# Performance work log

Measured on AMD Instinct MI355X. Metric: run time of the kernel, lower is better.

Reference implementation:

```python
import jax, jax.numpy as jnp
import numpy as np

N, E, B = 20000, 100000, 16
U_SZ, U_RED = 4096, 256
EDGE_H, EDGE_OUT = 1024, 512
NODE_H = 512
X_DIM, EA_DIM = 9, 1


def _lin(key, fan_out, fan_in):
    kw, kb = jax.random.split(key)
    s = 1.0 / np.sqrt(fan_in)
    w = jax.random.uniform(kw, (fan_out, fan_in), jnp.float32, -s, s)
    b = jax.random.uniform(kb, (fan_out,), jnp.float32, -s, s)
    return w, b


def setup_inputs() -> dict:
    key = jax.random.key(0)
    ks = jax.random.split(key, 16)
    inp = {}
    inp["x"] = jax.random.normal(ks[0], (N, X_DIM), jnp.float32)
    inp["edge_index"] = jax.random.randint(ks[1], (2, E), 0, N, jnp.int64)
    inp["edge_attr"] = jax.random.normal(ks[2], (E, EA_DIM), jnp.float32)
    inp["u"] = jax.random.normal(ks[3], (B, U_SZ), jnp.float32)
    inp["batch"] = jnp.sort(jax.random.randint(ks[4], (N,), 0, B, jnp.int64))
    # select_dim_reduction: Linear(4096, 256)
    inp["w_sel"], inp["b_sel"] = _lin(ks[5], U_RED, U_SZ)
    # edge MLP: 275 -> 1024 -> 1024 -> 1024 -> 1024 -> 512
    e_in = EA_DIM + 2 * X_DIM + U_RED  # 275
    inp["ew0"], inp["eb0"] = _lin(ks[6], EDGE_H, e_in)
    inp["ew1"], inp["eb1"] = _lin(ks[7], EDGE_H, EDGE_H)
    inp["ew2"], inp["eb2"] = _lin(ks[8], EDGE_H, EDGE_H)
    inp["ew3"], inp["eb3"] = _lin(ks[9], EDGE_H, EDGE_H)
    inp["ew4"], inp["eb4"] = _lin(ks[10], EDGE_OUT, EDGE_H)
    # node_mlp_1: (9+512) -> 512 -> 512 (relu after each)
    inp["nw0"], inp["nb0"] = _lin(ks[11], NODE_H, X_DIM + EDGE_OUT)
    inp["nw1"], inp["nb1"] = _lin(ks[12], NODE_H, NODE_H)
    # node_mlp_2: (9+512+256) -> 512 -> 1
    inp["mw0"], inp["mb0"] = _lin(ks[13], NODE_H, X_DIM + NODE_H + U_RED)
    inp["mw1"], inp["mb1"] = _lin(ks[14], 1, NODE_H)
    return inp


def reference(x, edge_index, edge_attr, u, batch,
              w_sel, b_sel,
              ew0, eb0, ew1, eb1, ew2, eb2, ew3, eb3, ew4, eb4,
              nw0, nb0, nw1, nb1, mw0, mb0, mw1, mb1):
    row, col = edge_index[0], edge_index[1]
    u_r = u @ w_sel.T + b_sel                       # [B, 256]
    eb_idx = batch[row]                             # edge -> graph
    # EdgeModel: cat([src, dest, edge_attr, u[batch]]) -> MLP
    e_in = jnp.concatenate([x[row], x[col], edge_attr, u_r[eb_idx]], axis=1)  # [E,275]
    h = jax.nn.relu(e_in @ ew0.T + eb0)
    h = jax.nn.relu(h @ ew1.T + eb1)
    h = jax.nn.relu(h @ ew2.T + eb2)
    h = jax.nn.relu(h @ ew3.T + eb3)
    edge_out = h @ ew4.T + eb4                      # [E, 512]
    # NodeModel: gather x[col], edge MLP, scatter_mean onto row
    n_in = jnp.concatenate([x[col], edge_out], axis=1)  # [E, 521]
    h = jax.nn.relu(n_in @ nw0.T + nb0)
    h = jax.nn.relu(h @ nw1.T + nb1)                # [E, 512]
    seg_sum = jax.ops.segment_sum(h, row, num_segments=x.shape[0])
    cnt = jax.ops.segment_sum(jnp.ones((h.shape[0],), h.dtype), row, num_segments=x.shape[0])
    agg = seg_sum / jnp.maximum(cnt, 1.0)[:, None]  # scatter_mean
    m_in = jnp.concatenate([x, agg, u_r[batch]], axis=1)  # [N, 777]
    h2 = jax.nn.relu(m_in @ mw0.T + mb0)
    out = h2 @ mw1.T + mb1                          # [N, 1]
    return jnp.squeeze(out)
```

## Files before the change

### kernel.cpp

```cpp
#include <hip/hip_runtime.h>


#define NN 20000
#define EE 100000
#define BB 16

typedef _Float16 f16x8 __attribute__((ext_vector_type(8)));
typedef _Float16 f16x4 __attribute__((ext_vector_type(4)));
typedef float f32x4 __attribute__((ext_vector_type(4)));

__device__ __forceinline__ int clampi(int v, int hi) {
    return v < 0 ? 0 : (v >= hi ? hi - 1 : v);
}

__device__ __forceinline__ void gld_lds16(const void* g, void* l) {
    __builtin_amdgcn_global_load_lds(
        (const __attribute__((address_space(1))) unsigned int*)g,
        (__attribute__((address_space(3))) unsigned int*)l, 16, 0, 0);
}

__global__ __launch_bounds__(512, 2) void gemm256(
    const _Float16* __restrict__ Ag, const _Float16* __restrict__ Wt,
    int KT, int KTs, const float* __restrict__ bias,
    _Float16* __restrict__ C, int KTo, int ktOff)
{
    __shared__ _Float16 As[32768];
    __shared__ _Float16 Bs[32768];

    const int tid  = threadIdx.x;
    const int lane = tid & 63;
    const int wid  = tid >> 6;
    const int wm = wid & 1;
    const int wn = wid >> 1;
    const int l15 = lane & 15;
    const int l4  = (lane >> 4) << 2;

    const int nb = gridDim.x;
    const int MT2 = gridDim.y;
    int f = blockIdx.y * nb + blockIdx.x;
    const int MT8 = MT2 & ~7;
    int p, c;
    if (f < MT8 * nb) {
        c = (f >> 3) % nb;
        p = (f & 7) + 8 * ((f >> 3) / nb);
    } else {
        int g = f - MT8 * nb;
        p = MT8 + g / nb;
        c = g % nb;
    }

    const int KTT = KT >> 1;
    const size_t soff = (size_t)tid * 8;
    const int doff = (tid & ~63) * 8;
    const int aoff = wm * 4096 + ((lane >> 4) << 10) + l15 * 8;
    const int boff = (wn >> 1) * 4096 + ((lane >> 4) << 10)
                   + ((wn & 1) * 64 + l15) * 8;

    auto stageA = [&](int tn, int s) {
        const size_t kk = (size_t)(2 * tn + s);
        const _Float16* g0 = Ag + ((size_t)(2 * p)     * KTs + kk) * 4096 + soff;
        const _Float16* g1 = Ag + ((size_t)(2 * p + 1) * KTs + kk) * 4096 + soff;
        _Float16* d = As + ((tn & 1) << 14) + (s << 13) + doff;
        gld_lds16(g0, d);
        gld_lds16(g1, d + 4096);
    };
    auto stageB = [&](int tn, int s) {
        const size_t kk = (size_t)(2 * tn + s);
        const _Float16* g0 = Wt + ((size_t)(2 * c)     * KT + kk) * 4096 + soff;
        const _Float16* g1 = Wt + ((size_t)(2 * c + 1) * KT + kk) * 4096 + soff;
        _Float16* d = Bs + ((tn & 1) << 14) + (s << 13) + doff;
        gld_lds16(g0, d);
        gld_lds16(g1, d + 4096);
    };

    f32x4 acc[8][4];
#pragma unroll
    for (int i = 0; i < 8; ++i)
#pragma unroll
        for (int j = 0; j < 4; ++j) acc[i][j] = (f32x4){0.f, 0.f, 0.f, 0.f};

    stageA(0, 0); stageB(0, 0); stageA(0, 1); stageB(0, 1);

    for (int t = 0; t < KTT; ++t) {
        const int pb = (t & 1) << 14;
#pragma unroll
        for (int sub = 0; sub < 2; ++sub) {
            if (t == KTT - 1 && sub == 1)
                asm volatile("s_waitcnt vmcnt(0)" ::: "memory");
            else
                asm volatile("s_waitcnt vmcnt(4)" ::: "memory");
            __builtin_amdgcn_s_barrier();
            const _Float16* Asub = As + pb + (sub << 13) + aoff;
            const _Float16* Bsub = Bs + pb + (sub << 13) + boff;
            f16x8 af[4], bf[4];
#pragma unroll
            for (int j = 0; j < 4; ++j) bf[j] = *(const f16x8*)(Bsub + j * 128);
#pragma unroll
            for (int i = 0; i < 4; ++i) af[i] = *(const f16x8*)(Asub + i * 128);
            if (t + 1 < KTT) stageA(t + 1, sub);
            __builtin_amdgcn_s_setprio(1);
#pragma unroll
            for (int i = 0; i < 4; ++i)
#pragma unroll
                for (int j = 0; j < 4; ++j)
                    acc[i][j] = __builtin_amdgcn_mfma_f32_16x16x32_f16(
                        af[i], bf[j], acc[i][j], 0, 0, 0);
            __builtin_amdgcn_s_setprio(0);
            __builtin_amdgcn_s_barrier();
#pragma unroll
            for (int i = 0; i < 4; ++i)
                af[i] = *(const f16x8*)(Asub + (4 + i) * 128);
            if (t + 1 < KTT) stageB(t + 1, sub);
            __builtin_amdgcn_s_setprio(1);
#pragma unroll
            for (int i = 0; i < 4; ++i)
#pragma unroll
                for (int j = 0; j < 4; ++j)
                    acc[4 + i][j] = __builtin_amdgcn_mfma_f32_16x16x32_f16(
                        af[i], bf[j], acc[4 + i][j], 0, 0, 0);
            __builtin_amdgcn_s_setprio(0);
        }
    }

    _Float16* tr = As;
#pragma unroll
    for (int pass = 0; pass < 4; ++pass) {
        __syncthreads();
        if (wm == (pass >> 1)) {
            const int fi = (pass & 1) << 2;
#pragma unroll
            for (int i = 0; i < 4; ++i) {
#pragma unroll
                for (int v = 0; v < 4; ++v) {
                    const int lr = i * 16 + l4 + v;
#pragma unroll
                    for (int j = 0; j < 4; ++j) {
                        const int cc = wn * 64 + j * 16 + l15;
                        float val = acc[fi + i][j][v] + bias[c * 256 + cc];
                        val = fmaxf(val, 0.f);
                        tr[lr * 264 + cc] = (_Float16)val;
                    }
                }
            }
        }
        __syncthreads();
#pragma unroll
        for (int it = 0; it < 4; ++it) {
            const int id = it * 512 + tid;
            const int r  = id & 63;
            const int cg = id >> 6;
            f16x8 v8 = *(const f16x8*)(tr + r * 264 + cg * 8);
            const int kt = ktOff + c * 8 + (cg >> 2);
            const int mt_out = 2 * p + (pass >> 1);
            const int r128 = ((pass & 1) << 6) + r;
            *(f16x8*)(C + (((size_t)mt_out * KTo + kt) * 4 + (cg & 3)) * 1024
                        + (size_t)r128 * 8) = v8;
        }
    }
}

template <int MODE>
__global__ __launch_bounds__(256, 4) void gemm_blk(
    const _Float16* __restrict__ A,
    const _Float16* __restrict__ Wt,
    int KT, int KTs,
    const float* __restrict__ bias, int ldbias, const int* __restrict__ gbid,
    void* __restrict__ C, int KTo, int ktOff,
    int ldc,
    const int* __restrict__ srow, float* __restrict__ aux,
    int M, int relu)
{
    __shared__ char smem[32768];
    _Float16* As = (_Float16*)smem;
    _Float16* Bs = As + 8192;

    const int tid  = threadIdx.x;
    const int lane = tid & 63;
    const int wid  = tid >> 6;
    const int wm = (wid & 1) << 6;
    const int wn = (wid >> 1) << 6;

    const int nb = gridDim.x;
    const int MT = gridDim.y;
    int f = blockIdx.y * nb + blockIdx.x;
    const int MT8 = MT & ~7;
    int p, c;
    if (f < MT8 * nb) {
        c = (f >> 3) % nb;
        p = (f & 7) + 8 * ((f >> 3) / nb);
    } else {
        int g = f - MT8 * nb;
        p = MT8 + g / nb;
        c = g % nb;
    }

    f32x4 acc[4][4];
#pragma unroll
    for (int i = 0; i < 4; ++i)
#pragma unroll
        for (int j = 0; j < 4; ++j) acc[i][j] = (f32x4){0.f, 0.f, 0.f, 0.f};

    const _Float16* pA = A + (size_t)p * KTs * 4096;
    const _Float16* pB = Wt + (size_t)c * KT * 4096;
    const int cb0 = wid * 64;
    const int cb1 = 256 + wid * 64;
    const int kq  = (lane >> 4) * 128;
    const int l15 = lane & 15;
    const int l4  = (lane >> 4) << 2;

    int kt = 0;
    for (; kt + 2 <= KT; kt += 2) {
        __syncthreads();
        gld_lds16(pA + (size_t)(cb0 + lane) * 8,        As + cb0 * 8);
        gld_lds16(pA + (size_t)(cb1 + lane) * 8,        As + cb1 * 8);
        gld_lds16(pA + 4096 + (size_t)(cb0 + lane) * 8, As + 4096 + cb0 * 8);
        gld_lds16(pA + 4096 + (size_t)(cb1 + lane) * 8, As + 4096 + cb1 * 8);
        gld_lds16(pB + (size_t)(cb0 + lane) * 8,        Bs + cb0 * 8);
        gld_lds16(pB + (size_t)(cb1 + lane) * 8,        Bs + cb1 * 8);
        gld_lds16(pB + 4096 + (size_t)(cb0 + lane) * 8, Bs + 4096 + cb0 * 8);
        gld_lds16(pB + 4096 + (size_t)(cb1 + lane) * 8, Bs + 4096 + cb1 * 8);
        pA += 8192; pB += 8192;
        __syncthreads();

#pragma unroll
        for (int s = 0; s < 2; ++s) {
            f16x8 af[4], bf[4];
            const int sb = s * 4096;
#pragma unroll
            for (int i = 0; i < 4; ++i)
                af[i] = *(const f16x8*)(As + sb + (size_t)((kq + wm + i * 16 + l15) << 3));
#pragma unroll
            for (int j = 0; j < 4; ++j)
                bf[j] = *(const f16x8*)(Bs + sb + (size_t)((kq + wn + j * 16 + l15) << 3));
#pragma unroll
            for (int i = 0; i < 4; ++i)
#pragma unroll
                for (int j = 0; j < 4; ++j)
                    acc[i][j] = __builtin_amdgcn_mfma_f32_16x16x32_f16(af[i], bf[j], acc[i][j], 0, 0, 0);
        }
    }
    if (kt < KT) {
        __syncthreads();
        gld_lds16(pA + (size_t)(cb0 + lane) * 8, As + cb0 * 8);
        gld_lds16(pA + (size_t)(cb1 + lane) * 8, As + cb1 * 8);
        gld_lds16(pB + (size_t)(cb0 + lane) * 8, Bs + cb0 * 8);
        gld_lds16(pB + (size_t)(cb1 + lane) * 8, Bs + cb1 * 8);
        __syncthreads();
        f16x8 af[4], bf[4];
#pragma unroll
        for (int i = 0; i < 4; ++i)
            af[i] = *(const f16x8*)(As + (size_t)((kq + wm + i * 16 + l15) << 3));
#pragma unroll
        for (int j = 0; j < 4; ++j)
            bf[j] = *(const f16x8*)(Bs + (size_t)((kq + wn + j * 16 + l15) << 3));
#pragma unroll
        for (int i = 0; i < 4; ++i)
#pragma unroll
            for (int j = 0; j < 4; ++j)
                acc[i][j] = __builtin_amdgcn_mfma_f32_16x16x32_f16(af[i], bf[j], acc[i][j], 0, 0, 0);
    }

    if (MODE == 0) {
        _Float16* tr = (_Float16*)smem;
#pragma unroll
        for (int pass = 0; pass < 2; ++pass) {
            __syncthreads();
            if (wm == pass * 64) {
#pragma unroll
                for (int i = 0; i < 4; ++i) {
#pragma unroll
                    for (int v = 0; v < 4; ++v) {
                        const int lr = i * 16 + l4 + v;
                        const float* brow = bias;
                        if (gbid) {
                            int m = p * 128 + pass * 64 + lr;
                            if (m >= M) m = M - 1;
                            brow = bias + (size_t)clampi(gbid[m], BB) * ldbias;
                        }
#pragma unroll
                        for (int j = 0; j < 4; ++j) {
                            const int cc = wn + j * 16 + l15;
                            float val = acc[i][j][v] + brow[c * 128 + cc];
                            if (relu) val = fmaxf(val, 0.f);
                            tr[lr * 132 + cc] = (_Float16)val;
                        }
                    }
                }
            }
            __syncthreads();
#pragma unroll
            for (int it = 0; it < 4; ++it) {
                const int id = it * 256 + tid;
                const int r  = id & 63;
                const int cg = id >> 6;
                f16x4 lo = *(const f16x4*)(tr + r * 132 + cg * 8);
                f16x4 hi = *(const f16x4*)(tr + r * 132 + cg * 8 + 4);
                f16x8 v8;
#pragma unroll
                for (int t = 0; t < 4; ++t) { v8[t] = lo[t]; v8[t + 4] = hi[t]; }
                const int kti = ktOff + (c << 2) + (cg >> 2);
                const int gr  = pass * 64 + r;
                size_t o = (((size_t)p * KTo + kti) * 4 + (cg & 3)) * 1024 + (size_t)gr * 8;
                *(f16x8*)((_Float16*)C + o) = v8;
            }
        }
    } else if (MODE == 1) {
#pragma unroll
        for (int i = 0; i < 4; ++i) {
#pragma unroll
            for (int v = 0; v < 4; ++v) {
                const int m = p * 128 + wm + i * 16 + l4 + v;
                if (m >= M) continue;
                const float* brow = bias;
                if (gbid) brow = bias + (size_t)clampi(gbid[m], BB) * ldbias;
#pragma unroll
                for (int j = 0; j < 4; ++j) {
                    const int col = c * 128 + wn + j * 16 + l15;
                    float val = acc[i][j][v] + brow[col];
                    if (relu) val = fmaxf(val, 0.f);
                    ((float*)C)[(size_t)m * ldc + col] = val;
                }
            }
        }
    } else if (MODE == 2) {
        float* trf = (float*)smem;
#pragma unroll
        for (int pass = 0; pass < 4; ++pass) {
            __syncthreads();
            if (wm == ((pass >> 1) << 6)) {
                const int i0 = (pass & 1) << 1;
#pragma unroll
                for (int ii = 0; ii < 2; ++ii) {
                    const int i = i0 + ii;
                    const int lr = ii * 16 + l4;
#pragma unroll
                    for (int v = 0; v < 4; ++v) {
#pragma unroll
                        for (int j = 0; j < 4; ++j) {
                            const int cc = wn + j * 16 + l15;
                            float val = acc[i][j][v] + bias[c * 128 + cc];
                            if (relu) val = fmaxf(val, 0.f);
                            trf[(lr + v) * 130 + cc] = val;
                        }
                    }
                }
            }
            __syncthreads();
            const int ebase = p * 128 + pass * 32;
#pragma unroll
            for (int it = 0; it < 16; ++it) {
                const int id = it * 256 + tid;
                const int lr = id >> 7;
                const int colg = id & 127;
                const int el = ebase + lr;
                if (el < M) {
                    const int node = clampi(srow[el], NN);
                    atomicAdd(&aux[(size_t)node * 512 + c * 128 + colg],
                              trf[lr * 130 + colg]);
                }
            }
        }
    } else {
        const float* mw1 = aux;
        float* out = (float*)C;
#pragma unroll
        for (int i = 0; i < 4; ++i) {
#pragma unroll
            for (int v = 0; v < 4; ++v) {
                const int m = p * 128 + wm + i * 16 + l4 + v;
                const int mc = m < M ? m : M - 1;
                const float* brow = bias + (size_t)clampi(gbid[mc], BB) * ldbias;
                float s = 0.f;
#pragma unroll
                for (int j = 0; j < 4; ++j) {
                    const int col = c * 128 + wn + j * 16 + l15;
                    float val = acc[i][j][v] + brow[col];
                    val = fmaxf(val, 0.f);
                    s += val * mw1[col];
                }
                s += __shfl_down(s, 8, 16);
                s += __shfl_down(s, 4, 16);
                s += __shfl_down(s, 2, 16);
                s += __shfl_down(s, 1, 16);
                if (l15 == 0 && m < M) atomicAdd(&out[m], s);
            }
        }
    }
}


__global__ void k_w2h_blk(const float* __restrict__ src, _Float16* __restrict__ dst,
                          int N, int Ksrc, int Kd, int mode)
{
    int t = blockIdx.x * blockDim.x + threadIdx.x;
    if (t >= N * Kd) return;
    int n = t / Kd, k = t - n * Kd;
    float v = 0.f;
    if (mode == 0)      { if (k < Ksrc) v = src[(size_t)n * Ksrc + k]; }
    else if (mode == 1) { if (k < 19) v = src[(size_t)n * 275 + k]; }
    else if (mode == 2) { if (k < 9) v = src[(size_t)n * Ksrc + k];
                          else if (k >= 32 && k < 544) v = src[(size_t)n * Ksrc + 9 + (k - 32)]; }
    else if (mode == 4) { if (k < Ksrc) v = src[(size_t)k * N + n]; }
    else                { v = src[(size_t)n * Ksrc + 9 + k]; }
    int KT = Kd >> 5;
    int nt = n >> 7, r = n & 127, kt = k >> 5, kg = (k >> 3) & 3, ko = k & 7;
    dst[(((size_t)nt * KT + kt) * 4 + kg) * 1024 + (size_t)r * 8 + ko] = (_Float16)v;
}

__global__ void k_fill_w32(const float* __restrict__ nw0, _Float16* __restrict__ whnc)
{
    int t = blockIdx.x * blockDim.x + threadIdx.x;
    if (t >= 512 * 32) return;
    int n = t >> 5, k = t & 31;
    float v = (k < 9) ? nw0[(size_t)n * 521 + k] : 0.f;
    int nt = n >> 7, r = n & 127, kg = (k >> 3) & 3, ko = k & 7;
    whnc[(((size_t)nt * 33 + 32) * 4 + kg) * 1024 + (size_t)r * 8 + ko] = (_Float16)v;
}

__global__ void k_bfuse(const float* __restrict__ nw0, const float* __restrict__ eb4,
                        const float* __restrict__ nb0, float* __restrict__ bf)
{
    int wave = (blockIdx.x * 256 + threadIdx.x) >> 6;
    int lane = threadIdx.x & 63;
    if (wave >= 512) return;
    const float* wr = nw0 + (size_t)wave * 521 + 9;
    float s = 0.f;
#pragma unroll
    for (int i = 0; i < 8; ++i) s += wr[lane * 8 + i] * eb4[lane * 8 + i];
    for (int off = 32; off; off >>= 1) s += __shfl_down(s, off);
    if (lane == 0) bf[wave] = s + nb0[wave];
}

__global__ void k_u_r(const float* __restrict__ u, const float* __restrict__ w_sel,
                      const float* __restrict__ b_sel, float* __restrict__ u_r)
{
    int wave = (blockIdx.x * 256 + threadIdx.x) >> 6;
    int lane = threadIdx.x & 63;
    int b = wave >> 8, n = wave & 255;
    const float4* u4 = (const float4*)(u + (size_t)b * 4096);
    const float4* w4 = (const float4*)(w_sel + (size_t)n * 4096);
    float s = 0.f;
    for (int i = lane; i < 1024; i += 64) {
        float4 a = u4[i], c = w4[i];
        s += a.x * c.x + a.y * c.y + a.z * c.z + a.w * c.w;
    }
    for (int off = 32; off; off >>= 1) s += __shfl_down(s, off);
    if (lane == 0) u_r[b * 256 + n] = s + b_sel[n];
}

__global__ void k_graph_bias(const float* __restrict__ u_r, const float* __restrict__ w,
                             const float* __restrict__ b, float* __restrict__ ub,
                             int Nout, int Ksrc, int koff)
{
    int wave = (blockIdx.x * 256 + threadIdx.x) >> 6;
    int lane = threadIdx.x & 63;
    if (wave >= 16 * Nout) return;
    int g = wave / Nout, n = wave - g * Nout;
    const float* ur = u_r + (size_t)g * 256;
    const float* wr = w + (size_t)n * Ksrc + koff;
    float s = 0.f;
#pragma unroll
    for (int i = 0; i < 4; ++i) s += ur[lane * 4 + i] * wr[lane * 4 + i];
    for (int off = 32; off; off >>= 1) s += __shfl_down(s, off);
    if (lane == 0) ub[(size_t)g * Nout + n] = s + b[n];
}

__global__ void k_gbe(const int* __restrict__ row, const int* __restrict__ batch,
                      int* __restrict__ gbe, float* __restrict__ cnt)
{
    int e = blockIdx.x * blockDim.x + threadIdx.x;
    if (e >= EE) return;
    int r = clampi(row[e], NN);
    gbe[e] = clampi(batch[r], BB);
    atomicAdd(&cnt[r], 1.f);
}

__global__ void k_init_out(float* __restrict__ out, const float* __restrict__ mb1)
{
    int t = blockIdx.x * blockDim.x + threadIdx.x;
    if (t < NN) out[t] = mb1[0];
}

__global__ void k_gather_edge_blk(const float* __restrict__ x, const float* __restrict__ ea,
                                  const int* __restrict__ row, const int* __restrict__ col,
                                  _Float16* __restrict__ dst, _Float16* __restrict__ pong,
                                  int e0, int ec, int MTR)
{
    int t = blockIdx.x * blockDim.x + threadIdx.x;
    if (t >= MTR * 4) return;
    int r = t >> 2, kg = t & 3;
    int e = e0 + r; int emax = e0 + ec - 1;
    if (e > emax) e = emax;
    int ri = clampi(row[e], NN), ci = clampi(col[e], NN);
    f16x8 v;
    f16x8 vx = (f16x8)(_Float16)0.f;
#pragma unroll
    for (int j = 0; j < 8; ++j) {
        int cc = kg * 8 + j;
        float fv = 0.f;
        if (cc < 9)       fv = x[(size_t)ri * 9 + cc];
        else if (cc < 18) fv = x[(size_t)ci * 9 + (cc - 9)];
        else if (cc == 18) fv = ea[e];
        v[j] = (_Float16)fv;
        if (cc < 9) vx[j] = (_Float16)x[(size_t)ci * 9 + cc];
    }
    *(f16x8*)(dst + (size_t)(r >> 7) * 4096 + (size_t)kg * 1024 + (size_t)(r & 127) * 8) = v;
    *(f16x8*)(pong + (((size_t)(r >> 7) * 33 + 32) * 4 + kg) * 1024 + (size_t)(r & 127) * 8) = vx;
}

__global__ void k_gather_min(const float* __restrict__ x, const float* __restrict__ agg,
                             const float* __restrict__ cnt, _Float16* __restrict__ dst, int MTR)
{
    int t = blockIdx.x * blockDim.x + threadIdx.x;
    if (t >= MTR * 68) return;
    int r = t / 68, q = t - r * 68;
    int kt = q >> 2, kg = q & 3;
    int n = r < NN ? r : NN - 1;
    f16x8 v = (f16x8)(_Float16)0.f;
    if (kt == 0) {
#pragma unroll
        for (int j = 0; j < 8; ++j) {
            int cc = kg * 8 + j;
            if (cc < 9) v[j] = (_Float16)x[(size_t)n * 9 + cc];
        }
    } else {
        float inv = 1.f / fmaxf(cnt[n], 1.f);
        int cbase = (kt - 1) * 32 + kg * 8;
        const float4* ap = (const float4*)(agg + (size_t)n * 512 + cbase);
        float4 a0 = ap[0], a1 = ap[1];
        v[0] = (_Float16)(a0.x * inv); v[1] = (_Float16)(a0.y * inv);
        v[2] = (_Float16)(a0.z * inv); v[3] = (_Float16)(a0.w * inv);
        v[4] = (_Float16)(a1.x * inv); v[5] = (_Float16)(a1.y * inv);
        v[6] = (_Float16)(a1.z * inv); v[7] = (_Float16)(a1.w * inv);
    }
    *(f16x8*)(dst + ((size_t)(r >> 7) * 17 + kt) * 4096 + (size_t)kg * 1024 + (size_t)(r & 127) * 8) = v;
}


#define GRID1(n) dim3(((n) + 255) / 256)

static inline void gemmB0(hipStream_t s, const _Float16* A, const _Float16* Wt, int KT, int KTs,
                          const float* bias, int ldbias, const int* gbid,
                          void* C, int KTo, int ktOff,
                          int M, int MT, int NT, int relu)
{
    hipLaunchKernelGGL(gemm_blk<0>, dim3(NT, MT), dim3(256), 0, s,
                       A, Wt, KT, KTs, bias, ldbias, gbid, C, KTo, ktOff, 0,
                       nullptr, nullptr, M, relu);
}
static inline void gemmB2(hipStream_t s, const _Float16* A, const _Float16* Wt, int KT, int KTs,
                          const float* bias, const int* srow, float* agg,
                          int M, int MT, int NT, int relu)
{
    hipLaunchKernelGGL(gemm_blk<2>, dim3(NT, MT), dim3(256), 0, s,
                       A, Wt, KT, KTs, bias, 0, nullptr, nullptr, 0, 0, 0,
                       srow, agg, M, relu);
}
static inline void gemmB3(hipStream_t s, const _Float16* A, const _Float16* Wt, int KT, int KTs,
                          const float* bias, int ldbias, const int* gbid,
                          float* out, const float* mw1,
                          int M, int MT, int NT)
{
    hipLaunchKernelGGL(gemm_blk<3>, dim3(NT, MT), dim3(256), 0, s,
                       A, Wt, KT, KTs, bias, ldbias, gbid, out, 0, 0, 0,
                       nullptr, (float*)mw1, M, 1);
}

extern "C" void kernel_launch(void* const* d_in, const int* in_sizes, int n_in,
                              void* d_out, int out_size, void* d_ws, size_t ws_size,
                              hipStream_t stream)
{
    const float* x     = (const float*)d_in[0];
    const int*   ei    = (const int*)d_in[1];
    const float* ea    = (const float*)d_in[2];
    const float* u     = (const float*)d_in[3];
    const int*   batch = (const int*)d_in[4];
    const float* w_sel = (const float*)d_in[5];
    const float* b_sel = (const float*)d_in[6];
    const float* ew0 = (const float*)d_in[7];   const float* eb0 = (const float*)d_in[8];
    const float* ew1 = (const float*)d_in[9];   const float* eb1 = (const float*)d_in[10];
    const float* ew2 = (const float*)d_in[11];  const float* eb2 = (const float*)d_in[12];
    const float* ew3 = (const float*)d_in[13];  const float* eb3 = (const float*)d_in[14];
    const float* ew4 = (const float*)d_in[15];  const float* eb4 = (const float*)d_in[16];
    const float* nw0 = (const float*)d_in[17];  const float* nb0 = (const float*)d_in[18];
    const float* nw1 = (const float*)d_in[19];  const float* nb1 = (const float*)d_in[20];
    const float* mw0 = (const float*)d_in[21];  const float* mb0 = (const float*)d_in[22];
    const float* mw1 = (const float*)d_in[23];  const float* mb1 = (const float*)d_in[24];

    const int* row = ei;
    const int* col = ei + EE;

    char* W = (char*)d_ws;
    size_t off = 0;
    auto alloc = [&](size_t bytes) -> char* {
        char* p = W + off;
        off = (off + bytes + 255) & ~(size_t)255;
        return p;
    };
    float*    cnt   = (float*)alloc(20000 * 4);
    float*    agg   = (float*)alloc((size_t)NN * 512 * 4);
    float*    zbias = (float*)alloc(1024 * 4);
    const size_t zeroBytes = off;
    float*    u_r  = (float*)alloc(16 * 256 * 4);
    float*    ub0  = (float*)alloc(16 * 1024 * 4);
    float*    ubm  = (float*)alloc(16 * 512 * 4);
    float*    bfu  = (float*)alloc(512 * 4);
    int*      gbe  = (int*)alloc((size_t)EE * 4);
    _Float16* wh0   = (_Float16*)alloc((size_t)8 * 1 * 4096 * 2);
    _Float16* wh1   = (_Float16*)alloc((size_t)8 * 32 * 4096 * 2);
    _Float16* wh2   = (_Float16*)alloc((size_t)8 * 32 * 4096 * 2);
    _Float16* wh3   = (_Float16*)alloc((size_t)8 * 32 * 4096 * 2);
    _Float16* whnc  = (_Float16*)alloc((size_t)4 * 33 * 4096 * 2);
    _Float16* whn1  = (_Float16*)alloc((size_t)4 * 16 * 4096 * 2);
    _Float16* whm0  = (_Float16*)alloc((size_t)4 * 17 * 4096 * 2);
    _Float16* nw0eoB= (_Float16*)alloc((size_t)4 * 16 * 4096 * 2);
    _Float16* ew4T  = (_Float16*)alloc((size_t)8 * 16 * 4096 * 2);
    const int MTm = (NN + 127) / 128;
    _Float16* m_in = (_Float16*)alloc((size_t)MTm * 17 * 4096 * 2);
    const size_t fixedBytes = off;

    static const int ecOpts[] = {50000, 25000, 12500, 10000, 5000};
    int EC = 5000;
    for (int i = 0; i < 5; ++i) {
        int ec = ecOpts[i];
        size_t MTRc = (size_t)((ec + 255) / 256) * 256;
        size_t need = fixedBytes + MTRc * 64 + 2 * (MTRc * 2112) + 4096;
        if (need <= ws_size) { EC = ec; break; }
    }
    const size_t MTR = (size_t)((EC + 255) / 256) * 256;
    const int MT  = (int)(MTR / 128);
    const int MT2 = (int)(MTR / 256);
    _Float16* e_in = (_Float16*)alloc(MTR * 64);
    _Float16* ping = (_Float16*)alloc(MTR * 2112);
    _Float16* pong = (_Float16*)alloc(MTR * 2112);
    const int NCH = (EE + EC - 1) / EC;

    (void)hipMemsetAsync(W, 0, zeroBytes, stream);
    hipLaunchKernelGGL(k_init_out, GRID1(NN), dim3(256), 0, stream, (float*)d_out, mb1);

    hipLaunchKernelGGL(k_u_r, dim3(1024), dim3(256), 0, stream, u, w_sel, b_sel, u_r);
    hipLaunchKernelGGL(k_graph_bias, GRID1(16 * 1024 * 64), dim3(256), 0, stream,
                       u_r, ew0, eb0, ub0, 1024, 275, 19);
    hipLaunchKernelGGL(k_graph_bias, GRID1(16 * 512 * 64), dim3(256), 0, stream,
                       u_r, mw0, mb0, ubm, 512, 777, 521);
    hipLaunchKernelGGL(k_gbe, GRID1(EE), dim3(256), 0, stream, row, batch, gbe, cnt);
    hipLaunchKernelGGL(k_bfuse, dim3(128), dim3(256), 0, stream, nw0, eb4, nb0, bfu);

    auto pack = [&](const float* w, _Float16* wh, int N, int Ksrc, int Kd, int mode) {
        hipLaunchKernelGGL(k_w2h_blk, GRID1(N * Kd), dim3(256), 0, stream, w, wh, N, Ksrc, Kd, mode);
    };
    pack(ew0, wh0, 1024, 275, 32, 1);
    pack(ew1, wh1, 1024, 1024, 1024, 0);
    pack(ew2, wh2, 1024, 1024, 1024, 0);
    pack(ew3, wh3, 1024, 1024, 1024, 0);
    pack(nw1, whn1, 512, 512, 512, 0);
    pack(mw0, whm0, 512, 777, 544, 2);
    pack(nw0, nw0eoB, 512, 521, 512, 5);
    pack(ew4, ew4T, 1024, 512, 512, 4);
    gemmB0(stream, nw0eoB, ew4T, 16, 16, zbias, 0, nullptr, whnc, 33, 0, 512, 4, 8, 0);
    hipLaunchKernelGGL(k_fill_w32, GRID1(512 * 32), dim3(256), 0, stream, nw0, whnc);

    for (int ch = 0; ch < NCH; ++ch) {
        int e0 = ch * EC;
        int ec = EC; if (e0 + ec > EE) ec = EE - e0;
        hipLaunchKernelGGL(k_gather_edge_blk, GRID1((int)MTR * 4), dim3(256), 0, stream,
                           x, ea, row, col, e_in, pong, e0, ec, (int)MTR);
        gemmB0(stream, e_in, wh0, 1, 1, ub0, 1024, gbe + e0, ping, 33, 0, ec, MT, 8, 1);
        hipLaunchKernelGGL(gemm256, dim3(4, MT2), dim3(512), 0, stream,
                           ping, wh1, 32, 33, eb1, pong, 33, 0);
        hipLaunchKernelGGL(gemm256, dim3(4, MT2), dim3(512), 0, stream,
                           pong, wh2, 32, 33, eb2, ping, 33, 0);
        hipLaunchKernelGGL(gemm256, dim3(4, MT2), dim3(512), 0, stream,
                           ping, wh3, 32, 33, eb3, pong, 33, 0);
        gemmB0(stream, pong, whnc, 33, 33, bfu, 0, nullptr, ping, 16, 0, ec, MT, 4, 1);
        gemmB2(stream, ping, whn1, 16, 16, nb1, row + e0, agg, ec, MT, 4, 1);
    }

    hipLaunchKernelGGL(k_gather_min, GRID1((int)(MTm * 128) * 68), dim3(256), 0, stream,
                       x, agg, cnt, m_in, MTm * 128);
    gemmB3(stream, m_in, whm0, 17, 17, ubm, 512, batch, (float*)d_out, mw1, NN, MTm, 4);
}
```

Measured before the change: 1.524 ms.

## Shrink big GEMM tile to 256x128 with 256 threads, reuse for fused node layer

Replaces the 256x256-tile, 512-thread GEMM with a 256x128-tile, 256-thread variant. It uses a simpler single-step double-buffered K loop and smaller shared-memory buffers, and launches twice as many column blocks. The same kernel now also runs the fused ew4/nw0 layer in place of the generic blocked GEMM. Smaller tiles may raise occupancy and spread work more evenly across CUs, but each tile reuses loaded data less and the pipeline overlaps loads less finely.

```diff
diff --git a/kernel.cpp b/kernel.cpp
--- a/kernel.cpp
+++ b/kernel.cpp
@@ -19,23 +19,23 @@
         (__attribute__((address_space(3))) unsigned int*)l, 16, 0, 0);
 }
 
-__global__ __launch_bounds__(512, 2) void gemm256(
+__global__ __launch_bounds__(256, 2) void gemm256n(
     const _Float16* __restrict__ Ag, const _Float16* __restrict__ Wt,
     int KT, int KTs, const float* __restrict__ bias,
     _Float16* __restrict__ C, int KTo, int ktOff)
 {
-    __shared__ _Float16 As[32768];
-    __shared__ _Float16 Bs[32768];
+    __shared__ _Float16 As[16384];
+    __shared__ _Float16 Bs[8192];
 
     const int tid  = threadIdx.x;
     const int lane = tid & 63;
     const int wid  = tid >> 6;
-    const int wm = wid & 1;
-    const int wn = wid >> 1;
-    const int l15 = lane & 15;
-    const int l4  = (lane >> 4) << 2;
-
-    const int nb = gridDim.x;
+    const int wm   = wid & 1;
+    const int wn   = wid >> 1;
+    const int l15  = lane & 15;
+    const int l4   = (lane >> 4) << 2;
+
+    const int nb  = gridDim.x;
     const int MT2 = gridDim.y;
     int f = blockIdx.y * nb + blockIdx.x;
     const int MT8 = MT2 & ~7;
@@ -49,77 +49,65 @@
         c = g % nb;
     }
 
-    const int KTT = KT >> 1;
-    const size_t soff = (size_t)tid * 8;
-    const int doff = (tid & ~63) * 8;
-    const int aoff = wm * 4096 + ((lane >> 4) << 10) + l15 * 8;
-    const int boff = (wn >> 1) * 4096 + ((lane >> 4) << 10)
-                   + ((wn & 1) * 64 + l15) * 8;
-
-    auto stageA = [&](int tn, int s) {
-        const size_t kk = (size_t)(2 * tn + s);
-        const _Float16* g0 = Ag + ((size_t)(2 * p)     * KTs + kk) * 4096 + soff;
-        const _Float16* g1 = Ag + ((size_t)(2 * p + 1) * KTs + kk) * 4096 + soff;
-        _Float16* d = As + ((tn & 1) << 14) + (s << 13) + doff;
-        gld_lds16(g0, d);
-        gld_lds16(g1, d + 4096);
+    f32x4 acc[8][4];
+#pragma unroll
+    for (int i = 0; i < 8; ++i)
+#pragma unroll
+        for (int j = 0; j < 4; ++j) acc[i][j] = (f32x4){0.f, 0.f, 0.f, 0.f};
+
+    const int kg = (lane >> 4) << 10;
+
+    auto stage = [&](int kt) {
+        const int par = (kt & 1);
+        const _Float16* a0 = Ag + ((size_t)(2 * p)     * KTs + kt) * 4096 + tid * 8;
+        const _Float16* a1 = Ag + ((size_t)(2 * p + 1) * KTs + kt) * 4096 + tid * 8;
+        const _Float16* b0 = Wt + ((size_t)c * KT + kt) * 4096 + tid * 8;
+        _Float16* dA = As + par * 8192 + wid * 512;
+        _Float16* dB = Bs + par * 4096 + wid * 512;
+        gld_lds16(a0,        dA);
+        gld_lds16(a0 + 2048, dA + 2048);
+        gld_lds16(a1,        dA + 4096);
+        gld_lds16(a1 + 2048, dA + 6144);
+        gld_lds16(b0,        dB);
+        gld_lds16(b0 + 2048, dB + 2048);
     };
-    auto stageB = [&](int tn, int s) {
-        const size_t kk = (size_t)(2 * tn + s);
-        const _Float16* g0 = Wt + ((size_t)(2 * c)     * KT + kk) * 4096 + soff;
-        const _Float16* g1 = Wt + ((size_t)(2 * c + 1) * KT + kk) * 4096 + soff;
-        _Float16* d = Bs + ((tn & 1) << 14) + (s << 13) + doff;
-        gld_lds16(g0, d);
-        gld_lds16(g1, d + 4096);
-    };
-
-    f32x4 acc[8][4];
-#pragma unroll
-    for (int i = 0; i < 8; ++i)
-#pragma unroll
-        for (int j = 0; j < 4; ++j) acc[i][j] = (f32x4){0.f, 0.f, 0.f, 0.f};
-
-    stageA(0, 0); stageB(0, 0); stageA(0, 1); stageB(0, 1);
-
-    for (int t = 0; t < KTT; ++t) {
-        const int pb = (t & 1) << 14;
-#pragma unroll
-        for (int sub = 0; sub < 2; ++sub) {
-            if (t == KTT - 1 && sub == 1)
-                asm volatile("s_waitcnt vmcnt(0)" ::: "memory");
-            else
-                asm volatile("s_waitcnt vmcnt(4)" ::: "memory");
-            __builtin_amdgcn_s_barrier();
-            const _Float16* Asub = As + pb + (sub << 13) + aoff;
-            const _Float16* Bsub = Bs + pb + (sub << 13) + boff;
-            f16x8 af[4], bf[4];
-#pragma unroll
-            for (int j = 0; j < 4; ++j) bf[j] = *(const f16x8*)(Bsub + j * 128);
-#pragma unroll
-            for (int i = 0; i < 4; ++i) af[i] = *(const f16x8*)(Asub + i * 128);
-            if (t + 1 < KTT) stageA(t + 1, sub);
-            __builtin_amdgcn_s_setprio(1);
-#pragma unroll
-            for (int i = 0; i < 4; ++i)
-#pragma unroll
-                for (int j = 0; j < 4; ++j)
-                    acc[i][j] = __builtin_amdgcn_mfma_f32_16x16x32_f16(
-                        af[i], bf[j], acc[i][j], 0, 0, 0);
-            __builtin_amdgcn_s_setprio(0);
-            __builtin_amdgcn_s_barrier();
-#pragma unroll
-            for (int i = 0; i < 4; ++i)
-                af[i] = *(const f16x8*)(Asub + (4 + i) * 128);
-            if (t + 1 < KTT) stageB(t + 1, sub);
-            __builtin_amdgcn_s_setprio(1);
-#pragma unroll
-            for (int i = 0; i < 4; ++i)
-#pragma unroll
-                for (int j = 0; j < 4; ++j)
-                    acc[4 + i][j] = __builtin_amdgcn_mfma_f32_16x16x32_f16(
-                        af[i], bf[j], acc[4 + i][j], 0, 0, 0);
-            __builtin_amdgcn_s_setprio(0);
-        }
+
+    stage(0);
+    for (int kt = 0; kt < KT; ++kt) {
+        if (kt + 1 < KT) {
+            stage(kt + 1);
+            asm volatile("s_waitcnt vmcnt(6)" ::: "memory");
+        } else {
+            asm volatile("s_waitcnt vmcnt(0)" ::: "memory");
+        }
+        __builtin_amdgcn_s_barrier();
+        const int par = (kt & 1);
+        const _Float16* Ap = As + par * 8192 + wm * 4096 + kg + l15 * 8;
+        const _Float16* Bp = Bs + par * 4096 + kg + (wn * 64 + l15) * 8;
+        f16x8 af[4], bf[4];
+#pragma unroll
+        for (int j = 0; j < 4; ++j) bf[j] = *(const f16x8*)(Bp + j * 128);
+#pragma unroll
+        for (int i = 0; i < 4; ++i) af[i] = *(const f16x8*)(Ap + i * 128);
+        __builtin_amdgcn_s_setprio(1);
+#pragma unroll
+        for (int i = 0; i < 4; ++i)
+#pragma unroll
+            for (int j = 0; j < 4; ++j)
+                acc[i][j] = __builtin_amdgcn_mfma_f32_16x16x32_f16(
+                    af[i], bf[j], acc[i][j], 0, 0, 0);
+        __builtin_amdgcn_s_setprio(0);
+#pragma unroll
+        for (int i = 0; i < 4; ++i) af[i] = *(const f16x8*)(Ap + (4 + i) * 128);
+        __builtin_amdgcn_s_setprio(1);
+#pragma unroll
+        for (int i = 0; i < 4; ++i)
+#pragma unroll
+            for (int j = 0; j < 4; ++j)
+                acc[4 + i][j] = __builtin_amdgcn_mfma_f32_16x16x32_f16(
+                    af[i], bf[j], acc[4 + i][j], 0, 0, 0);
+        __builtin_amdgcn_s_setprio(0);
+        __builtin_amdgcn_s_barrier();
     }
 
     _Float16* tr = As;
@@ -136,9 +124,9 @@
 #pragma unroll
                     for (int j = 0; j < 4; ++j) {
                         const int cc = wn * 64 + j * 16 + l15;
-                        float val = acc[fi + i][j][v] + bias[c * 256 + cc];
+                        float val = acc[fi + i][j][v] + bias[c * 128 + cc];
                         val = fmaxf(val, 0.f);
-                        tr[lr * 264 + cc] = (_Float16)val;
+                        tr[lr * 132 + cc] = (_Float16)val;
                     }
                 }
             }
@@ -146,14 +134,18 @@
         __syncthreads();
 #pragma unroll
         for (int it = 0; it < 4; ++it) {
-            const int id = it * 512 + tid;
+            const int id = it * 256 + tid;
             const int r  = id & 63;
             const int cg = id >> 6;
-            f16x8 v8 = *(const f16x8*)(tr + r * 264 + cg * 8);
-            const int kt = ktOff + c * 8 + (cg >> 2);
+            f16x4 lo = *(const f16x4*)(tr + r * 132 + cg * 8);
+            f16x4 hi = *(const f16x4*)(tr + r * 132 + cg * 8 + 4);
+            f16x8 v8;
+#pragma unroll
+            for (int t = 0; t < 4; ++t) { v8[t] = lo[t]; v8[t + 4] = hi[t]; }
+            const int kti = ktOff + c * 4 + (cg >> 2);
             const int mt_out = 2 * p + (pass >> 1);
             const int r128 = ((pass & 1) << 6) + r;
-            *(f16x8*)(C + (((size_t)mt_out * KTo + kt) * 4 + (cg & 3)) * 1024
+            *(f16x8*)(C + (((size_t)mt_out * KTo + kti) * 4 + (cg & 3)) * 1024
                         + (size_t)r128 * 8) = v8;
         }
     }
@@ -666,13 +658,14 @@
         hipLaunchKernelGGL(k_gather_edge_blk, GRID1((int)MTR * 4), dim3(256), 0, stream,
                            x, ea, row, col, e_in, pong, e0, ec, (int)MTR);
         gemmB0(stream, e_in, wh0, 1, 1, ub0, 1024, gbe + e0, ping, 33, 0, ec, MT, 8, 1);
-        hipLaunchKernelGGL(gemm256, dim3(4, MT2), dim3(512), 0, stream,
+        hipLaunchKernelGGL(gemm256n, dim3(8, MT2), dim3(256), 0, stream,
                            ping, wh1, 32, 33, eb1, pong, 33, 0);
-        hipLaunchKernelGGL(gemm256, dim3(4, MT2), dim3(512), 0, stream,
+        hipLaunchKernelGGL(gemm256n, dim3(8, MT2), dim3(256), 0, stream,
                            pong, wh2, 32, 33, eb2, ping, 33, 0);
-        hipLaunchKernelGGL(gemm256, dim3(4, MT2), dim3(512), 0, stream,
+        hipLaunchKernelGGL(gemm256n, dim3(8, MT2), dim3(256), 0, stream,
                            ping, wh3, 32, 33, eb3, pong, 33, 0);
-        gemmB0(stream, pong, whnc, 33, 33, bfu, 0, nullptr, ping, 16, 0, ec, MT, 4, 1);
+        hipLaunchKernelGGL(gemm256n, dim3(4, MT2), dim3(256), 0, stream,
+                           pong, whnc, 33, 33, bfu, ping, 16, 0);
         gemmB2(stream, ping, whn1, 16, 16, nb1, row + e0, agg, ec, MT, 4, 1);
     }
 
```

After: 1.614 ms. 5.9% more time.

## Add 128x128 pipelined GEMM kernel, resize edge chunks, and right-size per-chunk grids

Applied to the files above, without the earlier changes.

Adds a 256-thread gemmAD kernel with 128x128 tiles that streams A into LDS through a 4-slot ring of direct global-to-LDS loads and double-buffers B fragments in registers. It is used for the fused ew4/nw0 layer and for the wide hidden layers when the chunk is not the largest size. The first chunk-size option drops from 50000 to 32768, and grid sizes are now computed from each chunk's actual edge count, so the final partial chunk no longer launches padding tiles. The smaller chunk means more launches, and the smaller-tile kernel may get less data reuse per tile than gemm256.

```diff
diff --git a/kernel.cpp b/kernel.cpp
--- a/kernel.cpp
+++ b/kernel.cpp
@@ -155,6 +155,131 @@
             const int r128 = ((pass & 1) << 6) + r;
             *(f16x8*)(C + (((size_t)mt_out * KTo + kt) * 4 + (cg & 3)) * 1024
                         + (size_t)r128 * 8) = v8;
+        }
+    }
+}
+
+__global__ __launch_bounds__(256, 3) void gemmAD(
+    const _Float16* __restrict__ Ag, const _Float16* __restrict__ Wt,
+    int KT, int KTs, const float* __restrict__ bias,
+    _Float16* __restrict__ C, int KTo, int ktOff)
+{
+    __shared__ _Float16 As[16384];
+
+    const int tid  = threadIdx.x;
+    const int lane = tid & 63;
+    const int wid  = tid >> 6;
+    const int wm = (wid & 1) << 6;
+    const int wn = (wid >> 1) << 6;
+    const int l15 = lane & 15;
+    const int l4  = (lane >> 4) << 2;
+    const int kg  = (lane >> 4) << 10;
+
+    const int nb = gridDim.x;
+    const int MT = gridDim.y;
+    int f = blockIdx.y * nb + blockIdx.x;
+    const int MT8 = MT & ~7;
+    int p, c;
+    if (f < MT8 * nb) {
+        c = (f >> 3) % nb;
+        p = (f & 7) + 8 * ((f >> 3) / nb);
+    } else {
+        int g = f - MT8 * nb;
+        p = MT8 + g / nb;
+        c = g % nb;
+    }
+
+    f32x4 acc[4][4];
+#pragma unroll
+    for (int i = 0; i < 4; ++i)
+#pragma unroll
+        for (int j = 0; j < 4; ++j) acc[i][j] = (f32x4){0.f, 0.f, 0.f, 0.f};
+
+    const _Float16* gA = Ag + (size_t)p * KTs * 4096;
+    const _Float16* gB = Wt + ((size_t)c * KT) * 4096 + kg + (wn + l15) * 8;
+    const int ktLim = KT - 1;
+
+    auto stageA = [&](int ktA) {
+        const _Float16* s = gA + (size_t)ktA * 4096 + tid * 8;
+        _Float16* d = As + ((ktA & 3) << 12) + wid * 512;
+        gld_lds16(s, d);
+        gld_lds16(s + 2048, d + 2048);
+    };
+
+    f16x8 bfA[4], bfB[4];
+    auto loadB = [&](f16x8 (&bf)[4], int ktB) {
+        const _Float16* bp = gB + (size_t)ktB * 4096;
+#pragma unroll
+        for (int j = 0; j < 4; ++j) bf[j] = *(const f16x8*)(bp + j * 128);
+    };
+
+    stageA(0);
+    stageA(1 <= ktLim ? 1 : ktLim);
+    loadB(bfA, 0);
+
+    auto body = [&](int kt, f16x8 (&cur)[4], f16x8 (&nxt)[4]) {
+        const int ktB = kt + 1 <= ktLim ? kt + 1 : ktLim;
+        const int ktA = kt + 2 <= ktLim ? kt + 2 : ktLim;
+        loadB(nxt, ktB);
+        stageA(ktA);
+        asm volatile("s_waitcnt vmcnt(12)" ::: "memory");
+        __builtin_amdgcn_s_barrier();
+        asm volatile("" ::: "memory");
+        const _Float16* Ap = As + ((kt & 3) << 12) + kg + (wm + l15) * 8;
+        f16x8 af[4];
+#pragma unroll
+        for (int i = 0; i < 4; ++i) af[i] = *(const f16x8*)(Ap + i * 128);
+        __builtin_amdgcn_s_setprio(1);
+#pragma unroll
+        for (int i = 0; i < 4; ++i)
+#pragma unroll
+            for (int j = 0; j < 4; ++j)
+                acc[i][j] = __builtin_amdgcn_mfma_f32_16x16x32_f16(
+                    af[i], cur[j], acc[i][j], 0, 0, 0);
+        __builtin_amdgcn_s_setprio(0);
+    };
+
+    for (int kt = 0; kt + 2 <= KT; kt += 2) {
+        body(kt,     bfA, bfB);
+        body(kt + 1, bfB, bfA);
+    }
+    if (KT & 1) body(KT - 1, bfA, bfB);
+
+    _Float16* tr = As;
+#pragma unroll
+    for (int pass = 0; pass < 2; ++pass) {
+        __syncthreads();
+        if (wm == pass * 64) {
+#pragma unroll
+            for (int i = 0; i < 4; ++i) {
+#pragma unroll
+                for (int v = 0; v < 4; ++v) {
+                    const int lr = i * 16 + l4 + v;
+#pragma unroll
+                    for (int j = 0; j < 4; ++j) {
+                        const int cc = wn + j * 16 + l15;
+                        float val = acc[i][j][v] + bias[c * 128 + cc];
+                        val = fmaxf(val, 0.f);
+                        tr[lr * 132 + cc] = (_Float16)val;
+                    }
+                }
+            }
+        }
+        __syncthreads();
+#pragma unroll
+        for (int it = 0; it < 4; ++it) {
+            const int id = it * 256 + tid;
+            const int r  = id & 63;
+            const int cg = id >> 6;
+            f16x4 lo = *(const f16x4*)(tr + r * 132 + cg * 8);
+            f16x4 hi = *(const f16x4*)(tr + r * 132 + cg * 8 + 4);
+            f16x8 v8;
+#pragma unroll
+            for (int t = 0; t < 4; ++t) { v8[t] = lo[t]; v8[t + 4] = hi[t]; }
+            const int kti = ktOff + (c << 2) + (cg >> 2);
+            const int gr  = pass * 64 + r;
+            size_t o = (((size_t)p * KTo + kti) * 4 + (cg & 3)) * 1024 + (size_t)gr * 8;
+            *(f16x8*)(C + o) = v8;
         }
     }
 }
@@ -619,7 +744,7 @@
     _Float16* m_in = (_Float16*)alloc((size_t)MTm * 17 * 4096 * 2);
     const size_t fixedBytes = off;
 
-    static const int ecOpts[] = {50000, 25000, 12500, 10000, 5000};
+    static const int ecOpts[] = {32768, 25000, 12500, 10000, 5000};
     int EC = 5000;
     for (int i = 0; i < 5; ++i) {
         int ec = ecOpts[i];
@@ -627,9 +752,8 @@
         size_t need = fixedBytes + MTRc * 64 + 2 * (MTRc * 2112) + 4096;
         if (need <= ws_size) { EC = ec; break; }
     }
+    const bool big = (EC == 32768);
     const size_t MTR = (size_t)((EC + 255) / 256) * 256;
-    const int MT  = (int)(MTR / 128);
-    const int MT2 = (int)(MTR / 256);
     _Float16* e_in = (_Float16*)alloc(MTR * 64);
     _Float16* ping = (_Float16*)alloc(MTR * 2112);
     _Float16* pong = (_Float16*)alloc(MTR * 2112);
@@ -663,17 +787,27 @@
     for (int ch = 0; ch < NCH; ++ch) {
         int e0 = ch * EC;
         int ec = EC; if (e0 + ec > EE) ec = EE - e0;
-        hipLaunchKernelGGL(k_gather_edge_blk, GRID1((int)MTR * 4), dim3(256), 0, stream,
-                           x, ea, row, col, e_in, pong, e0, ec, (int)MTR);
-        gemmB0(stream, e_in, wh0, 1, 1, ub0, 1024, gbe + e0, ping, 33, 0, ec, MT, 8, 1);
-        hipLaunchKernelGGL(gemm256, dim3(4, MT2), dim3(512), 0, stream,
-                           ping, wh1, 32, 33, eb1, pong, 33, 0);
-        hipLaunchKernelGGL(gemm256, dim3(4, MT2), dim3(512), 0, stream,
-                           pong, wh2, 32, 33, eb2, ping, 33, 0);
-        hipLaunchKernelGGL(gemm256, dim3(4, MT2), dim3(512), 0, stream,
-                           ping, wh3, 32, 33, eb3, pong, 33, 0);
-        gemmB0(stream, pong, whnc, 33, 33, bfu, 0, nullptr, ping, 16, 0, ec, MT, 4, 1);
-        gemmB2(stream, ping, whn1, 16, 16, nb1, row + e0, agg, ec, MT, 4, 1);
+        const int ecr  = ((ec + 255) / 256) * 256;
+        const int MTc  = ecr / 128;
+        const int MT2c = ecr / 256;
+        hipLaunchKernelGGL(k_gather_edge_blk, GRID1(ecr * 4), dim3(256), 0, stream,
+                           x, ea, row, col, e_in, pong, e0, ec, ecr);
+        gemmB0(stream, e_in, wh0, 1, 1, ub0, 1024, gbe + e0, ping, 33, 0, ec, MTc, 8, 1);
+        auto wideL = [&](const _Float16* Ain, const _Float16* Wt,
+                         const float* b, _Float16* Cout) {
+            if (big)
+                hipLaunchKernelGGL(gemm256, dim3(4, MT2c), dim3(512), 0, stream,
+                                   Ain, Wt, 32, 33, b, Cout, 33, 0);
+            else
+                hipLaunchKernelGGL(gemmAD, dim3(8, MTc), dim3(256), 0, stream,
+                                   Ain, Wt, 32, 33, b, Cout, 33, 0);
+        };
+        wideL(ping, wh1, eb1, pong);
+        wideL(pong, wh2, eb2, ping);
+        wideL(ping, wh3, eb3, pong);
+        hipLaunchKernelGGL(gemmAD, dim3(4, MTc), dim3(256), 0, stream,
+                           pong, whnc, 33, 33, bfu, ping, 16, 0);
+        gemmB2(stream, ping, whn1, 16, 16, nb1, row + e0, agg, ec, MTc, 4, 1);
     }
 
     hipLaunchKernelGGL(k_gather_min, GRID1((int)(MTm * 128) * 68), dim3(256), 0, stream,
```

New measurement: 1.407 ms. 7.7% less time.
